# Optimization experiments

Hardware: AMD Instinct MI355X
Metric: run time of the kernel (lower is better)

## Reference

```python
import jax, jax.numpy as jnp
import numpy as np
import math

QDIM = 512
KDIM = 512
MID = 512
MAIN_N = 2048
OTHER_N = 2048
BATCH = 32
NEG_BIG = -float(1 << 32)


def setup_inputs() -> dict:
    key = jax.random.key(0)
    ks = jax.random.split(key, 8)
    main_feat = jax.random.normal(ks[0], (MAIN_N, QDIM), dtype=jnp.float32)
    other_feat = jax.random.normal(ks[1], (OTHER_N, KDIM), dtype=jnp.float32)
    fix_feat = jax.random.uniform(ks[2], (BATCH, OTHER_N), dtype=jnp.float32)
    mask = jax.random.randint(ks[3], (MAIN_N, OTHER_N), 0, 2).astype(bool)
    # Linear params (PyTorch layout: W [out, in], b [out])
    sq = 1.0 / math.sqrt(QDIM)
    sk = 1.0 / math.sqrt(KDIM)
    Wq = jax.random.uniform(ks[4], (MID, QDIM), jnp.float32, -sq, sq)
    bq = jax.random.uniform(ks[5], (MID,), jnp.float32, -sq, sq)
    Wk = jax.random.uniform(ks[6], (MID, KDIM), jnp.float32, -sk, sk)
    bk = jax.random.uniform(ks[7], (MID,), jnp.float32, -sk, sk)
    return {"main_feat": main_feat, "other_feat": other_feat, "fix_feat": fix_feat,
            "mask": mask, "Wq": Wq, "bq": bq, "Wk": Wk, "bk": bk}


def reference(main_feat, other_feat, fix_feat, mask, Wq, bq, Wk, bk):
    # Q: [main, mid], K: [other, mid]
    Q = main_feat @ Wq.T + bq
    K = other_feat @ Wk.T + bk
    attn = (Q @ K.T) / math.sqrt(MID)            # [main, other]
    attn = jnp.where(mask, NEG_BIG, attn)
    attn = jax.nn.softmax(attn, axis=-1)
    # diag_embed(fix_feat) @ other_feat == per-token broadcast scale
    scaled = fix_feat[:, :, None] * other_feat[None, :, :]   # [batch, other, Kdim]
    return jnp.einsum('mo,bok->bmk', attn, scaled)           # [batch, main, Kdim]
```

## Files before the change

kernel.cpp:

```cpp
#include <hip/hip_runtime.h>
#include <hip/hip_bf16.h>

typedef unsigned short u16;
typedef __attribute__((ext_vector_type(8))) short short8;
typedef __attribute__((ext_vector_type(4))) float f32x4;

#define BATCH_ 32

static __device__ __forceinline__ float b2f(u16 u) {
  union { unsigned int i; float f; } v; v.i = ((unsigned int)u) << 16; return v.f;
}
static __device__ __forceinline__ u16 f2b(float x) {
  unsigned int i = __float_as_uint(x);
  unsigned int r = (i + 0x7fffu + ((i >> 16) & 1u)) >> 16;
  return (u16)r;
}

#define GCAST(p) ((const __attribute__((address_space(1))) void*)(p))
#define LCAST(p) ((__attribute__((address_space(3))) void*)(p))

__global__ __launch_bounds__(256) void cvt_bf16(const float* __restrict__ src,
                                                u16* __restrict__ dst, int n) {
  int i = (blockIdx.x * 256 + threadIdx.x) * 4;
  if (i >= n) return;
  float4 v = *(const float4*)(src + i);
  ushort4 o;
  o.x = f2b(v.x); o.y = f2b(v.y); o.z = f2b(v.z); o.w = f2b(v.w);
  *(ushort4*)(dst + i) = o;
}

__global__ __launch_bounds__(256) void transpose_cvt(const float* __restrict__ src,
                                                     u16* __restrict__ dst, int R, int C) {
  __shared__ float tile[32][33];
  int c0 = blockIdx.x * 32, r0 = blockIdx.y * 32;
  int tx = threadIdx.x & 31, ty = threadIdx.x >> 5;
  #pragma unroll
  for (int i = 0; i < 32; i += 8)
    tile[ty + i][tx] = src[(long long)(r0 + ty + i) * C + c0 + tx];
  __syncthreads();
  #pragma unroll
  for (int i = 0; i < 32; i += 8)
    dst[(long long)(c0 + ty + i) * R + r0 + tx] = f2b(tile[tx][ty + i]);
}

__global__ __launch_bounds__(256) void build_scaled(const u16* __restrict__ oT,
                                                    const float* __restrict__ fix,
                                                    u16* __restrict__ out) {
  long long i4 = (long long)blockIdx.x * 256 + threadIdx.x;
  int o = (int)(i4 & 511) * 4;
  long long bk = i4 >> 9;
  int b = (int)(bk >> 9);
  int kk = (int)(bk & 511);
  ushort4 v = *(const ushort4*)(oT + (long long)kk * 2048 + o);
  float4 f = *(const float4*)(fix + (long long)b * 2048 + o);
  ushort4 r;
  r.x = f2b(b2f(v.x) * f.x); r.y = f2b(b2f(v.y) * f.y);
  r.z = f2b(b2f(v.z) * f.z); r.w = f2b(b2f(v.w) * f.w);
  *(ushort4*)(out + bk * 2048 + o) = r;
}

__global__ __launch_bounds__(256) void softmax_mask(const float* __restrict__ S,
                                                    const int* __restrict__ mask,
                                                    u16* __restrict__ P, int N) {
  const float scale = 0.044194173824159216f;
  int row = blockIdx.x;
  int t = threadIdx.x;
  long long base = (long long)row * N;
  float vals[8]; int msk[8];
  float mx = -3.0e38f;
  #pragma unroll
  for (int i = 0; i < 8; ++i) {
    int c = t + i * 256;
    float s = S[base + c] * scale;
    int m = mask[base + c];
    vals[i] = s; msk[i] = m;
    if (!m) mx = fmaxf(mx, s);
  }
  #pragma unroll
  for (int off = 32; off; off >>= 1) mx = fmaxf(mx, __shfl_xor(mx, off));
  __shared__ float sred[4];
  if ((t & 63) == 0) sred[t >> 6] = mx;
  __syncthreads();
  mx = fmaxf(fmaxf(sred[0], sred[1]), fmaxf(sred[2], sred[3]));
  __syncthreads();
  float e[8]; float sum = 0.f;
  #pragma unroll
  for (int i = 0; i < 8; ++i) {
    e[i] = msk[i] ? 0.f : __expf(vals[i] - mx);
    sum += e[i];
  }
  #pragma unroll
  for (int off = 32; off; off >>= 1) sum += __shfl_xor(sum, off);
  if ((t & 63) == 0) sred[t >> 6] = sum;
  __syncthreads();
  sum = sred[0] + sred[1] + sred[2] + sred[3];
  float inv = (sum > 0.f) ? (1.f / sum) : 0.f;
  #pragma unroll
  for (int i = 0; i < 8; ++i) {
    int c = t + i * 256;
    P[base + c] = f2b(e[i] * inv);
  }
}

#define GBM 128
#define GBN 128
#define GBK 32

template<int EPI>
__global__ __launch_bounds__(256) void gemm_lds(
    const u16* __restrict__ A, const u16* __restrict__ Bt,
    const float* __restrict__ bias,
    const u16* __restrict__ Bt2, const float* __restrict__ bias2,
    float* __restrict__ outF, u16* __restrict__ outB,
    int M, int N, int K) {
  __shared__ u16 sA[GBM * GBK];
  __shared__ u16 sB[GBN * GBK];
  int m0 = blockIdx.y * GBM, n0 = blockIdx.x * GBN;
  if (EPI == 0) {
    if (2 * blockIdx.y >= gridDim.y) { Bt = Bt2; bias = bias2; }
  }
  int t = threadIdx.x;
  int wid = t >> 6, lane = t & 63;
  int wm = (wid >> 1) * 64, wn = (wid & 1) * 64;
  int lr = lane & 15, lq = lane >> 4;
  int srow = lane >> 2, schunk = (lane & 3) * 8;

  f32x4 acc[4][4];
  #pragma unroll
  for (int i = 0; i < 4; ++i)
    #pragma unroll
    for (int j = 0; j < 4; ++j)
      acc[i][j] = (f32x4){0.f, 0.f, 0.f, 0.f};

  const u16* gA = A + (long long)(m0 + wid * 32 + srow) * K + schunk;
  const u16* gB = Bt + (long long)(n0 + wid * 32 + srow) * K + schunk;
  u16* lA = &sA[(wid * 32) * GBK];
  u16* lB = &sB[(wid * 32) * GBK];
  const long long rowskip = (long long)16 * K;

  for (int k0 = 0; k0 < K; k0 += GBK) {
    __builtin_amdgcn_global_load_lds(GCAST(gA + k0),           LCAST(lA),            16, 0, 0);
    __builtin_amdgcn_global_load_lds(GCAST(gA + k0 + rowskip), LCAST(lA + 16 * GBK), 16, 0, 0);
    __builtin_amdgcn_global_load_lds(GCAST(gB + k0),           LCAST(lB),            16, 0, 0);
    __builtin_amdgcn_global_load_lds(GCAST(gB + k0 + rowskip), LCAST(lB + 16 * GBK), 16, 0, 0);
    __syncthreads();
    short8 af[4], bf[4];
    #pragma unroll
    for (int i = 0; i < 4; ++i)
      af[i] = *(const short8*)&sA[(wm + i * 16 + lr) * GBK + lq * 8];
    #pragma unroll
    for (int j = 0; j < 4; ++j)
      bf[j] = *(const short8*)&sB[(wn + j * 16 + lr) * GBK + lq * 8];
    #pragma unroll
    for (int i = 0; i < 4; ++i)
      #pragma unroll
      for (int j = 0; j < 4; ++j)
        acc[i][j] = __builtin_amdgcn_mfma_f32_16x16x32_bf16(af[i], bf[j], acc[i][j], 0, 0, 0);
    __syncthreads();
  }

  #pragma unroll
  for (int i = 0; i < 4; ++i) {
    #pragma unroll
    for (int j = 0; j < 4; ++j) {
      int col = n0 + wn + j * 16 + lr;
      #pragma unroll
      for (int r = 0; r < 4; ++r) {
        int row = m0 + wm + i * 16 + lq * 4 + r;
        float v = acc[i][j][r];
        if (EPI == 0) {
          outB[(long long)row * N + col] = f2b(v + bias[col]);
        } else {
          outF[(long long)row * N + col] = v;
        }
      }
    }
  }
}

#define SGB __builtin_amdgcn_sched_group_barrier

__global__ __launch_bounds__(512, 2) void gemm_ring(
    const u16* __restrict__ A, const u16* __restrict__ Bt,
    float* __restrict__ outF, int M, int N, int K) {
  __shared__ u16 lds[4][2][8192];

  int nwg = gridDim.x * gridDim.y;
  int wg = blockIdx.y * gridDim.x + blockIdx.x;
  int cpx = nwg >> 3;
  int swz = (wg & 7) * cpx + (wg >> 3);
  int bx = swz & 7, by = swz >> 3;
  int m0 = bx * 256, n0 = by * 256;

  int t = threadIdx.x;
  int w = t >> 6, lane = t & 63;
  int wr = w >> 2, wc = w & 3;
  int lr = lane & 15, lq = lane >> 4;
  int csw = (((lr >> 1) & 3) ^ lq) * 8;

  int srow = t >> 2;
  int sgc = (((srow >> 1) & 3) ^ (t & 3)) * 8;
  const u16* pA0 = A + (long long)(m0 + srow) * K + sgc;
  const u16* pA1 = pA0 + (long long)128 * K;
  const u16* pB0 = Bt + (long long)(n0 + srow) * K + sgc;
  const u16* pB1 = pB0 + (long long)128 * K;
  const int lbase = (w * 16) * 32;

  f32x4 acc[8][4];
  #pragma unroll
  for (int i = 0; i < 8; ++i)
    #pragma unroll
    for (int j = 0; j < 4; ++j)
      acc[i][j] = (f32x4){0.f, 0.f, 0.f, 0.f};

  const int NT = K >> 5;

  #define STAGE_TILE(KT, SB)                                                          \
    do {                                                                              \
      long long cofs = (long long)(KT) * 32;                                          \
      __builtin_amdgcn_global_load_lds(GCAST(pA0 + cofs), LCAST(&lds[SB][0][lbase]),            16, 0, 0); \
      __builtin_amdgcn_global_load_lds(GCAST(pA1 + cofs), LCAST(&lds[SB][0][lbase + 128 * 32]), 16, 0, 0); \
      __builtin_amdgcn_global_load_lds(GCAST(pB0 + cofs), LCAST(&lds[SB][1][lbase]),            16, 0, 0); \
      __builtin_amdgcn_global_load_lds(GCAST(pB1 + cofs), LCAST(&lds[SB][1][lbase + 128 * 32]), 16, 0, 0); \
    } while (0)

  #define RD_FRAGS(AF, BF, BUF) {                                                     \
    _Pragma("unroll")                                                                 \
    for (int i = 0; i < 8; ++i)                                                       \
      AF[i] = *(const short8*)&lds[BUF][0][(wr * 128 + i * 16 + lr) * 32 + csw];      \
    _Pragma("unroll")                                                                 \
    for (int j = 0; j < 4; ++j)                                                       \
      BF[j] = *(const short8*)&lds[BUF][1][(wc * 64 + j * 16 + lr) * 32 + csw]; }

  #define MFMA_NP(AF, BF) {                                                           \
    _Pragma("unroll")                                                                 \
    for (int i = 0; i < 8; ++i)                                                       \
      _Pragma("unroll")                                                               \
      for (int j = 0; j < 4; ++j)                                                     \
        acc[i][j] = __builtin_amdgcn_mfma_f32_16x16x32_bf16(AF[i], BF[j], acc[i][j], 0, 0, 0); }

  #define MFMA_BLK(AF, BF) {                                                          \
    __builtin_amdgcn_s_setprio(1);                                                    \
    MFMA_NP(AF, BF);                                                                  \
    __builtin_amdgcn_s_setprio(0); }

  #define SGB_TAIL() {                                                                \
    SGB(0x008, 2, 0);                                                                 \
    SGB(0x100, 2, 0); SGB(0x008, 4, 0);                                               \
    SGB(0x100, 2, 0); SGB(0x008, 4, 0);                                               \
    SGB(0x100, 2, 0); SGB(0x008, 4, 0);                                               \
    SGB(0x020, 4, 0);                                                                 \
    SGB(0x100, 2, 0); SGB(0x008, 4, 0);                                               \
    SGB(0x100, 2, 0); SGB(0x008, 4, 0);                                               \
    SGB(0x100, 2, 0); SGB(0x008, 4, 0);                                               \
    SGB(0x008, 6, 0); }

  short8 afA[8], bfA[4], afB[8], bfB[4];

  STAGE_TILE(0, 0);
  STAGE_TILE(1, 1);
  STAGE_TILE(2, 2);
  asm volatile("s_waitcnt vmcnt(4)" ::: "memory");
  __builtin_amdgcn_s_barrier();
  __builtin_amdgcn_sched_barrier(0);
  RD_FRAGS(afA, bfA, 0);

  for (int kt = 0; kt + 4 < NT; kt += 2) {
    RD_FRAGS(afB, bfB, ((kt + 1) & 3));
    STAGE_TILE(kt + 3, ((kt + 3) & 3));
    MFMA_NP(afA, bfA);
    SGB_TAIL();
    asm volatile("s_waitcnt vmcnt(4)" ::: "memory");
    __builtin_amdgcn_s_barrier();
    __builtin_amdgcn_sched_barrier(0);
    RD_FRAGS(afA, bfA, ((kt + 2) & 3));
    STAGE_TILE(kt + 4, ((kt + 4) & 3));
    MFMA_NP(afB, bfB);
    SGB_TAIL();
    asm volatile("s_waitcnt vmcnt(4)" ::: "memory");
    __builtin_amdgcn_s_barrier();
    __builtin_amdgcn_sched_barrier(0);
  }

  RD_FRAGS(afB, bfB, ((NT - 3) & 3));
  STAGE_TILE(NT - 1, ((NT - 1) & 3));
  __builtin_amdgcn_sched_barrier(0);
  MFMA_BLK(afA, bfA);
  __builtin_amdgcn_sched_barrier(0);
  asm volatile("s_waitcnt vmcnt(4)" ::: "memory");
  __builtin_amdgcn_s_barrier();
  __builtin_amdgcn_sched_barrier(0);
  RD_FRAGS(afA, bfA, ((NT - 2) & 3));
  __builtin_amdgcn_sched_barrier(0);
  MFMA_BLK(afB, bfB);
  __builtin_amdgcn_sched_barrier(0);
  asm volatile("s_waitcnt vmcnt(0)" ::: "memory");
  __builtin_amdgcn_s_barrier();
  __builtin_amdgcn_sched_barrier(0);
  RD_FRAGS(afB, bfB, ((NT - 1) & 3));
  __builtin_amdgcn_sched_barrier(0);
  MFMA_BLK(afA, bfA);
  MFMA_BLK(afB, bfB);

  #undef STAGE_TILE
  #undef RD_FRAGS
  #undef MFMA_NP
  #undef MFMA_BLK
  #undef SGB_TAIL

  #pragma unroll
  for (int i = 0; i < 8; ++i) {
    #pragma unroll
    for (int j = 0; j < 4; ++j) {
      int col = n0 + wc * 64 + j * 16 + lr;
      int b = col >> 9, kc = col & 511;
      float* ob = outF + (long long)b * ((long long)M * 512) + kc;
      #pragma unroll
      for (int r = 0; r < 4; ++r) {
        int row = m0 + wr * 128 + i * 16 + lq * 4 + r;
        ob[(long long)row * 512] = acc[i][j][r];
      }
    }
  }
}

#define BMT 128
#define BNT 128
#define BKT 32
#define LDSP 40

template<int MODE>
__global__ __launch_bounds__(256) void gemm_bt(
    const u16* __restrict__ A, const u16* __restrict__ Bt,
    const float* __restrict__ bias, const float* __restrict__ fixmat,
    float* __restrict__ outF, u16* __restrict__ outB,
    int M, int N, int K, long long out_batch_stride, int bt_batch_stride) {
  __shared__ u16 sA[BMT][LDSP];
  __shared__ u16 sB[BNT][LDSP];
  int b = blockIdx.z;
  const u16* Bt_b = Bt + (long long)b * bt_batch_stride;
  const float* fixrow = (MODE == 2) ? (fixmat + (long long)b * K) : nullptr;
  float* out_b = (MODE != 0) ? (outF + (long long)b * out_batch_stride) : nullptr;

  int m0 = blockIdx.y * BMT, n0 = blockIdx.x * BNT;
  int t = threadIdx.x;
  int wid = t >> 6, lane = t & 63;
  int wm = (wid >> 1) * 64, wn = (wid & 1) * 64;
  int lr = lane & 15, lq = lane >> 4;

  f32x4 acc[4][4];
  #pragma unroll
  for (int i = 0; i < 4; ++i)
    #pragma unroll
    for (int j = 0; j < 4; ++j)
      acc[i][j] = (f32x4){0.f, 0.f, 0.f, 0.f};

  int srow = t >> 1, scg = (t & 1) * 16;

  for (int k0 = 0; k0 < K; k0 += BKT) {
    {
      const u16* src = A + (long long)(m0 + srow) * K + k0 + scg;
      short8 v0 = *(const short8*)(src);
      short8 v1 = *(const short8*)(src + 8);
      *(short8*)&sA[srow][scg] = v0;
      *(short8*)&sA[srow][scg + 8] = v1;
    }
    {
      const u16* src = Bt_b + (long long)(n0 + srow) * K + k0 + scg;
      short8 v0 = *(const short8*)(src);
      short8 v1 = *(const short8*)(src + 8);
      if (MODE == 2) {
        u16* p0 = (u16*)&v0; u16* p1 = (u16*)&v1;
        #pragma unroll
        for (int j = 0; j < 8; ++j) {
          p0[j] = f2b(b2f(p0[j]) * fixrow[k0 + scg + j]);
          p1[j] = f2b(b2f(p1[j]) * fixrow[k0 + scg + 8 + j]);
        }
      }
      *(short8*)&sB[srow][scg] = v0;
      *(short8*)&sB[srow][scg + 8] = v1;
    }
    __syncthreads();
    short8 af[4], bf[4];
    #pragma unroll
    for (int i = 0; i < 4; ++i)
      af[i] = *(const short8*)&sA[wm + i * 16 + lr][lq * 8];
    #pragma unroll
    for (int j = 0; j < 4; ++j)
      bf[j] = *(const short8*)&sB[wn + j * 16 + lr][lq * 8];
    #pragma unroll
    for (int i = 0; i < 4; ++i)
      #pragma unroll
      for (int j = 0; j < 4; ++j)
        acc[i][j] = __builtin_amdgcn_mfma_f32_16x16x32_bf16(af[i], bf[j], acc[i][j], 0, 0, 0);
    __syncthreads();
  }

  #pragma unroll
  for (int i = 0; i < 4; ++i) {
    #pragma unroll
    for (int j = 0; j < 4; ++j) {
      int col = n0 + wn + j * 16 + lr;
      #pragma unroll
      for (int r = 0; r < 4; ++r) {
        int row = m0 + wm + i * 16 + lq * 4 + r;
        float v = acc[i][j][r];
        if (MODE == 0) {
          v += bias[col];
          outB[(long long)row * N + col] = f2b(v);
        } else {
          out_b[(long long)row * N + col] = v;
        }
      }
    }
  }
}

extern "C" void kernel_launch(void* const* d_in, const int* in_sizes, int n_in,
                              void* d_out, int out_size, void* d_ws, size_t ws_size,
                              hipStream_t stream) {
  const float* main_feat  = (const float*)d_in[0];
  const float* other_feat = (const float*)d_in[1];
  const float* fix_feat   = (const float*)d_in[2];
  const int*   mask       = (const int*)d_in[3];
  const float* Wq         = (const float*)d_in[4];
  const float* bq         = (const float*)d_in[5];
  const float* Wk         = (const float*)d_in[6];
  const float* bk         = (const float*)d_in[7];
  float* out = (float*)d_out;

  char* ws = (char*)d_ws;
  const size_t OFF_MAINB  = 0;
  const size_t OFF_OTHERB = 2097152;
  const size_t OFF_WQB    = 4194304;
  const size_t OFF_WKB    = 4718592;
  const size_t OFF_QB     = 5242880;
  const size_t OFF_KB     = 7340032;
  const size_t OFF_OTB    = 9437184;
  const size_t OFF_P      = 11534336;
  const size_t OFF_S      = 19922944;
  const size_t OFF_SCALED = 36700160;
  const size_t NEED_SCALED = OFF_SCALED + (size_t)BATCH_ * 512 * 2048 * 2;

  u16* mainB  = (u16*)(ws + OFF_MAINB);
  u16* otherB = (u16*)(ws + OFF_OTHERB);
  u16* WqB    = (u16*)(ws + OFF_WQB);
  u16* WkB    = (u16*)(ws + OFF_WKB);
  u16* QB     = (u16*)(ws + OFF_QB);
  u16* KB     = (u16*)(ws + OFF_KB);
  u16* oTB    = (u16*)(ws + OFF_OTB);
  u16* P      = (u16*)(ws + OFF_P);
  float* S    = (float*)(ws + OFF_S);
  u16* scaled = (u16*)(ws + OFF_SCALED);
  bool use_scaled = (ws_size >= NEED_SCALED);

  cvt_bf16<<<1024, 256, 0, stream>>>(main_feat, mainB, 2048 * 512);
  cvt_bf16<<<1024, 256, 0, stream>>>(other_feat, otherB, 2048 * 512);
  cvt_bf16<<<256, 256, 0, stream>>>(Wq, WqB, 512 * 512);
  cvt_bf16<<<256, 256, 0, stream>>>(Wk, WkB, 512 * 512);
  transpose_cvt<<<dim3(16, 64), 256, 0, stream>>>(other_feat, oTB, 2048, 512);

  if (use_scaled) {
    gemm_lds<0><<<dim3(4, 32), 256, 0, stream>>>(mainB, WqB, bq, WkB, bk,
        nullptr, QB, 4096, 512, 512);
    gemm_lds<1><<<dim3(16, 16), 256, 0, stream>>>(QB, KB, nullptr, nullptr, nullptr,
        S, nullptr, 2048, 2048, 512);
    softmax_mask<<<2048, 256, 0, stream>>>(S, mask, P, 2048);
    build_scaled<<<32768, 256, 0, stream>>>(oTB, fix_feat, scaled);
    gemm_ring<<<dim3(8, 64), 512, 0, stream>>>(P, scaled, out, 2048, 16384, 2048);
  } else {
    gemm_bt<0><<<dim3(4, 16, 1), 256, 0, stream>>>(mainB, WqB, bq, nullptr,
        nullptr, QB, 2048, 512, 512, 0, 0);
    gemm_bt<0><<<dim3(4, 16, 1), 256, 0, stream>>>(otherB, WkB, bk, nullptr,
        nullptr, KB, 2048, 512, 512, 0, 0);
    gemm_bt<1><<<dim3(16, 16, 1), 256, 0, stream>>>(QB, KB, nullptr, nullptr,
        S, nullptr, 2048, 2048, 512, 0, 0);
    softmax_mask<<<2048, 256, 0, stream>>>(S, mask, P, 2048);
    gemm_bt<2><<<dim3(4, 16, BATCH_), 256, 0, stream>>>(P, oTB, nullptr, fix_feat,
        out, nullptr, 2048, 512, 2048, 1048576LL, 0);
  }
}
```

Baseline: 186.1 us.

## Fuse transpose with fix scaling, merge conversions, store scores in bf16

Builds the batch-scaled other_feat directly from the fp32 source in one transpose_scale kernel, so the separate transpose_cvt pass and the bf16 oT intermediate are no longer needed on the main path. Merges the four bf16 conversion launches into two dual-input launches. Writes the QK^T score matrix as bf16 instead of fp32 and reads it as bf16 in softmax, which halves that intermediate's traffic. The cost is lower precision on the attention logits before softmax. The transpose_scale write pattern (ushort2 stores) may also coalesce less well than the old build_scaled kernel.

```diff
diff --git a/kernel.cpp b/kernel.cpp
--- a/kernel.cpp
+++ b/kernel.cpp
@@ -19,47 +19,49 @@
 #define GCAST(p) ((const __attribute__((address_space(1))) void*)(p))
 #define LCAST(p) ((__attribute__((address_space(3))) void*)(p))
 
-__global__ __launch_bounds__(256) void cvt_bf16(const float* __restrict__ src,
-                                                u16* __restrict__ dst, int n) {
+__global__ __launch_bounds__(256) void cvt_bf16_dual(
+    const float* __restrict__ s1, u16* __restrict__ d1, int n1,
+    const float* __restrict__ s2, u16* __restrict__ d2, int n2) {
   int i = (blockIdx.x * 256 + threadIdx.x) * 4;
-  if (i >= n) return;
-  float4 v = *(const float4*)(src + i);
+  const float* s; u16* d; int idx;
+  if (i < n1) { s = s1; d = d1; idx = i; }
+  else { idx = i - n1; if (idx >= n2) return; s = s2; d = d2; }
+  float4 v = *(const float4*)(s + idx);
   ushort4 o;
   o.x = f2b(v.x); o.y = f2b(v.y); o.z = f2b(v.z); o.w = f2b(v.w);
-  *(ushort4*)(dst + i) = o;
-}
-
-__global__ __launch_bounds__(256) void transpose_cvt(const float* __restrict__ src,
-                                                     u16* __restrict__ dst, int R, int C) {
+  *(ushort4*)(d + idx) = o;
+}
+
+__global__ __launch_bounds__(256) void transpose_scale(
+    const float* __restrict__ other, const float* __restrict__ fix,
+    u16* __restrict__ scaled) {
   __shared__ float tile[32][33];
-  int c0 = blockIdx.x * 32, r0 = blockIdx.y * 32;
+  __shared__ float fixs[32][33];
+  int k0 = blockIdx.x * 32, o0 = blockIdx.y * 32;
   int tx = threadIdx.x & 31, ty = threadIdx.x >> 5;
   #pragma unroll
   for (int i = 0; i < 32; i += 8)
-    tile[ty + i][tx] = src[(long long)(r0 + ty + i) * C + c0 + tx];
+    tile[ty + i][tx] = other[(long long)(o0 + ty + i) * 512 + k0 + tx];
+  #pragma unroll
+  for (int i = 0; i < 32; i += 8)
+    fixs[ty + i][tx] = fix[(long long)(ty + i) * 2048 + o0 + tx];
   __syncthreads();
-  #pragma unroll
-  for (int i = 0; i < 32; i += 8)
-    dst[(long long)(c0 + ty + i) * R + r0 + tx] = f2b(tile[tx][ty + i]);
-}
-
-__global__ __launch_bounds__(256) void build_scaled(const u16* __restrict__ oT,
-                                                    const float* __restrict__ fix,
-                                                    u16* __restrict__ out) {
-  long long i4 = (long long)blockIdx.x * 256 + threadIdx.x;
-  int o = (int)(i4 & 511) * 4;
-  long long bk = i4 >> 9;
-  int b = (int)(bk >> 9);
-  int kk = (int)(bk & 511);
-  ushort4 v = *(const ushort4*)(oT + (long long)kk * 2048 + o);
-  float4 f = *(const float4*)(fix + (long long)b * 2048 + o);
-  ushort4 r;
-  r.x = f2b(b2f(v.x) * f.x); r.y = f2b(b2f(v.y) * f.y);
-  r.z = f2b(b2f(v.z) * f.z); r.w = f2b(b2f(v.w) * f.w);
-  *(ushort4*)(out + bk * 2048 + o) = r;
-}
-
-__global__ __launch_bounds__(256) void softmax_mask(const float* __restrict__ S,
+  int kk = threadIdx.x >> 4;
+  int oo = (threadIdx.x & 15) * 2;
+  #pragma unroll 4
+  for (int b = 0; b < 32; ++b) {
+    #pragma unroll
+    for (int p = 0; p < 2; ++p) {
+      int k = kk + p * 16;
+      ushort2 w;
+      w.x = f2b(tile[oo][k] * fixs[b][oo]);
+      w.y = f2b(tile[oo + 1][k] * fixs[b][oo + 1]);
+      *(ushort2*)(scaled + ((long long)(b * 512 + k0 + k) * 2048 + o0 + oo)) = w;
+    }
+  }
+}
+
+__global__ __launch_bounds__(256) void softmax_mask(const u16* __restrict__ S,
                                                     const int* __restrict__ mask,
                                                     u16* __restrict__ P, int N) {
   const float scale = 0.044194173824159216f;
@@ -71,7 +73,7 @@
   #pragma unroll
   for (int i = 0; i < 8; ++i) {
     int c = t + i * 256;
-    float s = S[base + c] * scale;
+    float s = b2f(S[base + c]) * scale;
     int m = mask[base + c];
     vals[i] = s; msk[i] = m;
     if (!m) mx = fmaxf(mx, s);
@@ -170,8 +172,10 @@
         float v = acc[i][j][r];
         if (EPI == 0) {
           outB[(long long)row * N + col] = f2b(v + bias[col]);
+        } else if (EPI == 1) {
+          outF[(long long)row * N + col] = v;
         } else {
-          outF[(long long)row * N + col] = v;
+          outB[(long long)row * N + col] = f2b(v);
         }
       }
     }
@@ -324,6 +328,20 @@
   }
 }
 
+__global__ __launch_bounds__(256) void transpose_cvt(const float* __restrict__ src,
+                                                     u16* __restrict__ dst, int R, int C) {
+  __shared__ float tile[32][33];
+  int c0 = blockIdx.x * 32, r0 = blockIdx.y * 32;
+  int tx = threadIdx.x & 31, ty = threadIdx.x >> 5;
+  #pragma unroll
+  for (int i = 0; i < 32; i += 8)
+    tile[ty + i][tx] = src[(long long)(r0 + ty + i) * C + c0 + tx];
+  __syncthreads();
+  #pragma unroll
+  for (int i = 0; i < 32; i += 8)
+    dst[(long long)(c0 + ty + i) * R + r0 + tx] = f2b(tile[tx][ty + i]);
+}
+
 #define BMT 128
 #define BNT 128
 #define BKT 32
@@ -340,7 +358,7 @@
   int b = blockIdx.z;
   const u16* Bt_b = Bt + (long long)b * bt_batch_stride;
   const float* fixrow = (MODE == 2) ? (fixmat + (long long)b * K) : nullptr;
-  float* out_b = (MODE != 0) ? (outF + (long long)b * out_batch_stride) : nullptr;
+  float* out_b = (MODE == 1 || MODE == 2) ? (outF + (long long)b * out_batch_stride) : nullptr;
 
   int m0 = blockIdx.y * BMT, n0 = blockIdx.x * BNT;
   int t = threadIdx.x;
@@ -408,6 +426,8 @@
         if (MODE == 0) {
           v += bias[col];
           outB[(long long)row * N + col] = f2b(v);
+        } else if (MODE == 3) {
+          outB[(long long)row * N + col] = f2b(v);
         } else {
           out_b[(long long)row * N + col] = v;
         }
@@ -450,31 +470,31 @@
   u16* KB     = (u16*)(ws + OFF_KB);
   u16* oTB    = (u16*)(ws + OFF_OTB);
   u16* P      = (u16*)(ws + OFF_P);
-  float* S    = (float*)(ws + OFF_S);
+  u16* S      = (u16*)(ws + OFF_S);
   u16* scaled = (u16*)(ws + OFF_SCALED);
   bool use_scaled = (ws_size >= NEED_SCALED);
 
-  cvt_bf16<<<1024, 256, 0, stream>>>(main_feat, mainB, 2048 * 512);
-  cvt_bf16<<<1024, 256, 0, stream>>>(other_feat, otherB, 2048 * 512);
-  cvt_bf16<<<256, 256, 0, stream>>>(Wq, WqB, 512 * 512);
-  cvt_bf16<<<256, 256, 0, stream>>>(Wk, WkB, 512 * 512);
-  transpose_cvt<<<dim3(16, 64), 256, 0, stream>>>(other_feat, oTB, 2048, 512);
+  cvt_bf16_dual<<<2048, 256, 0, stream>>>(main_feat, mainB, 2048 * 512,
+                                          other_feat, otherB, 2048 * 512);
+  cvt_bf16_dual<<<512, 256, 0, stream>>>(Wq, WqB, 512 * 512,
+                                         Wk, WkB, 512 * 512);
 
   if (use_scaled) {
+    transpose_scale<<<dim3(16, 64), 256, 0, stream>>>(other_feat, fix_feat, scaled);
     gemm_lds<0><<<dim3(4, 32), 256, 0, stream>>>(mainB, WqB, bq, WkB, bk,
         nullptr, QB, 4096, 512, 512);
-    gemm_lds<1><<<dim3(16, 16), 256, 0, stream>>>(QB, KB, nullptr, nullptr, nullptr,
-        S, nullptr, 2048, 2048, 512);
+    gemm_lds<3><<<dim3(16, 16), 256, 0, stream>>>(QB, KB, nullptr, nullptr, nullptr,
+        nullptr, S, 2048, 2048, 512);
     softmax_mask<<<2048, 256, 0, stream>>>(S, mask, P, 2048);
-    build_scaled<<<32768, 256, 0, stream>>>(oTB, fix_feat, scaled);
     gemm_ring<<<dim3(8, 64), 512, 0, stream>>>(P, scaled, out, 2048, 16384, 2048);
   } else {
+    transpose_cvt<<<dim3(16, 64), 256, 0, stream>>>(other_feat, oTB, 2048, 512);
     gemm_bt<0><<<dim3(4, 16, 1), 256, 0, stream>>>(mainB, WqB, bq, nullptr,
         nullptr, QB, 2048, 512, 512, 0, 0);
     gemm_bt<0><<<dim3(4, 16, 1), 256, 0, stream>>>(otherB, WkB, bk, nullptr,
         nullptr, KB, 2048, 512, 512, 0, 0);
-    gemm_bt<1><<<dim3(16, 16, 1), 256, 0, stream>>>(QB, KB, nullptr, nullptr,
-        S, nullptr, 2048, 2048, 512, 0, 0);
+    gemm_bt<3><<<dim3(16, 16, 1), 256, 0, stream>>>(QB, KB, nullptr, nullptr,
+        nullptr, S, 2048, 2048, 512, 0, 0);
     softmax_mask<<<2048, 256, 0, stream>>>(S, mask, P, 2048);
     gemm_bt<2><<<dim3(4, 16, BATCH_), 256, 0, stream>>>(P, oTB, nullptr, fix_feat,
         out, nullptr, 2048, 512, 2048, 1048576LL, 0);
```

After: 177.0 us. 4.9% less time.
